# Kernel optimization log

Hardware: AMD Instinct MI355X
Metric: run time of the kernel (lower is better)

## Reference

```python
import jax, jax.numpy as jnp
import numpy as np

N_NODES = 40000
N_EDGES = 640000
IN, HID, OUT = 128, 256, 47


def setup_inputs() -> dict:
    key = jax.random.key(0)
    ks = jax.random.split(key, 8)
    x = jax.random.normal(ks[0], (N_NODES, IN), dtype=jnp.float32)
    # PyTorch Linear(fan_in, fan_out): store as [fan_in, fan_out] for y = h @ W + b
    W1 = jax.random.normal(ks[1], (2 * IN, HID), dtype=jnp.float32) / np.sqrt(2 * IN)
    b1 = jnp.zeros((HID,), jnp.float32)
    W2 = jax.random.normal(ks[2], (2 * HID, HID), dtype=jnp.float32) / np.sqrt(2 * HID)
    b2 = jnp.zeros((HID,), jnp.float32)
    W3 = jax.random.normal(ks[3], (2 * HID, OUT), dtype=jnp.float32) / np.sqrt(2 * HID)
    b3 = jnp.zeros((OUT,), jnp.float32)
    src = jax.random.randint(ks[4], (N_EDGES,), 0, N_NODES, dtype=jnp.int64 if jax.config.jax_enable_x64 else jnp.int32)
    dst = jax.random.randint(ks[5], (N_EDGES,), 0, N_NODES, dtype=jnp.int64 if jax.config.jax_enable_x64 else jnp.int32)
    return {"x": x, "W1": W1, "b1": b1, "W2": W2, "b2": b2, "W3": W3, "b3": b3,
            "src": src, "dst": dst}


def _sage_layer(h, src, dst, W, b):
    # copy_u -> mean: gather src features, scatter-sum into dst, divide by in-degree
    msum = jax.ops.segment_sum(h[src], dst, num_segments=N_NODES)  # [N, d]
    deg = jax.ops.segment_sum(jnp.ones_like(dst, dtype=h.dtype), dst, num_segments=N_NODES)
    mean = msum / jnp.maximum(deg, 1.0)[:, None]  # zero-degree nodes get 0 (DGL mean convention)
    cat = jnp.concatenate([h, mean], axis=1)      # [N, 2d]
    return cat @ W + b


def reference(x, W1, b1, W2, b2, W3, b3, src, dst):
    # dropout is identity in eval mode
    h = jax.nn.relu(_sage_layer(x, src, dst, W1, b1))
    h = jax.nn.relu(_sage_layer(h, src, dst, W2, b2))
    return _sage_layer(h, src, dst, W3, b3)
```

## Files before the change

kernel.cpp:

```cpp
#include <hip/hip_runtime.h>

#define NNODES 40000
#define NEDGES 640000
#define DIN 128
#define DHID 256
#define DOUT 47
#define NCNT 40960
#define NPART (NCNT / 256)

typedef __attribute__((ext_vector_type(8))) short short8;
typedef __attribute__((ext_vector_type(4))) float f32x4;

#define GLD16(gp, lp)                                                        \
    __builtin_amdgcn_global_load_lds(                                        \
        (const __attribute__((address_space(1))) void*)(gp),                 \
        (__attribute__((address_space(3))) void*)(lp), 16, 0, 0)

__device__ inline float bf2f(unsigned short u) {
    union { unsigned int i; float f; } c; c.i = ((unsigned int)u) << 16; return c.f;
}
__device__ inline unsigned short f2bf(float f) {
    union { float f; unsigned int i; } c; c.f = f;
    unsigned int x = c.i;
    x += 0x7fff + ((x >> 16) & 1);
    return (unsigned short)(x >> 16);
}

__global__ void hist_kernel(const int* __restrict__ dst, int* __restrict__ cnt) {
    int t = blockIdx.x * blockDim.x + threadIdx.x;
    if (t < NEDGES) atomicAdd(&cnt[dst[t]], 1);
}

__global__ void part_kernel(const int* __restrict__ cnt, int* __restrict__ part) {
    int b = blockIdx.x, t = threadIdx.x;
    int v = cnt[b * 256 + t];
#pragma unroll
    for (int off = 32; off > 0; off >>= 1) v += __shfl_down(v, off);
    __shared__ int ws[4];
    if ((t & 63) == 0) ws[t >> 6] = v;
    __syncthreads();
    if (t == 0) part[b] = ws[0] + ws[1] + ws[2] + ws[3];
}

__global__ void writeptr_kernel(const int* __restrict__ cnt, const int* __restrict__ part,
                                int* __restrict__ rowptr) {
    __shared__ int shp[256];
    __shared__ int sh[256];
    int b = blockIdx.x, t = threadIdx.x;
    int pv = (t < NPART) ? part[t] : 0;
    shp[t] = pv;
    __syncthreads();
    for (int off = 1; off < 256; off <<= 1) {
        int add = (t >= off) ? shp[t - off] : 0;
        __syncthreads();
        shp[t] += add;
        __syncthreads();
    }
    int partoff = (b == 0) ? 0 : shp[b - 1];
    int idx = b * 256 + t;
    int v = cnt[idx];
    sh[t] = v;
    __syncthreads();
    for (int off = 1; off < 256; off <<= 1) {
        int add = (t >= off) ? sh[t - off] : 0;
        __syncthreads();
        sh[t] += add;
        __syncthreads();
    }
    rowptr[idx] = partoff + sh[t] - v;
}

__global__ void fill_kernel(const int* __restrict__ src, const int* __restrict__ dst,
                            const int* __restrict__ rowptr, int* __restrict__ fill,
                            unsigned short* __restrict__ eidx) {
    int e = blockIdx.x * blockDim.x + threadIdx.x;
    if (e < NEDGES) {
        int d = dst[e];
        int pos = rowptr[d] + atomicAdd(&fill[d], 1);
        eidx[pos] = (unsigned short)src[e];
    }
}

__global__ void conv_all_kernel(const float* __restrict__ x,
                                const float* __restrict__ W1,
                                const float* __restrict__ W2,
                                const float* __restrict__ W3,
                                unsigned short* __restrict__ xbf,
                                unsigned short* __restrict__ wt1,
                                unsigned short* __restrict__ wt2,
                                unsigned short* __restrict__ wt3,
                                int* __restrict__ czero) {
    const int N0 = NNODES * DIN / 4;
    const int N1 = 2 * DIN * DHID;
    const int N2 = 2 * DHID * DHID;
    const int N3 = 94 * 256;
    int t = blockIdx.x * blockDim.x + threadIdx.x;
    if (t < 2 * NCNT) czero[t] = 0;
    if (t < N0) {
        float4 v = ((const float4*)x)[t];
        ushort4 r;
        r.x = f2bf(v.x); r.y = f2bf(v.y); r.z = f2bf(v.z); r.w = f2bf(v.w);
        ((ushort4*)xbf)[t] = r;
    } else if (t < N0 + N1) {
        int u = t - N0;
        int k = u >> 8, n = u & 255;
        wt1[(size_t)n * 256 + k] = f2bf(W1[u]);
    } else if (t < N0 + N1 + N2) {
        int u = t - N0 - N1;
        int k = u >> 8, n = u & 255;
        wt2[(size_t)n * 512 + k] = f2bf(W2[u]);
    } else if (t < N0 + N1 + N2 + N3) {
        int u = t - N0 - N1 - N2;
        int n = u >> 8, k = u & 255;
        float v = (n < 47) ? W3[(size_t)k * DOUT + n]
                           : W3[(size_t)(k + DHID) * DOUT + (n - 47)];
        wt3[u] = f2bf(v);
    }
}

template <int D>
__global__ void agg_bf16_kernel(const unsigned short* __restrict__ h,
                                const int* __restrict__ rowptr,
                                const unsigned short* __restrict__ eidx,
                                unsigned short* __restrict__ mean) {
    constexpr int VPL = D / 64;
    const int node = blockIdx.x * (blockDim.x >> 6) + (threadIdx.x >> 6);
    if (node >= NNODES) return;
    const int lane = threadIdx.x & 63;
    const int beg = rowptr[node], end = rowptr[node + 1];
    const unsigned short* hp = h + lane * VPL;

    float acc[VPL];
#pragma unroll
    for (int i = 0; i < VPL; ++i) acc[i] = 0.0f;

    for (int base = beg; base < end; base += 64) {
        int n = min(64, end - base);
        int myidx = (base + lane < end) ? (int)eidx[base + lane] : 0;
        int j = 0;
        for (; j + 8 <= n; j += 8) {
            int s[8];
#pragma unroll
            for (int u = 0; u < 8; ++u) s[u] = __shfl(myidx, j + u);
            if constexpr (VPL == 4) {
                ushort4 v[8];
#pragma unroll
                for (int u = 0; u < 8; ++u) v[u] = *(const ushort4*)(hp + (size_t)s[u] * D);
#pragma unroll
                for (int u = 0; u < 8; ++u) {
                    acc[0] += bf2f(v[u].x); acc[1] += bf2f(v[u].y);
                    acc[2] += bf2f(v[u].z); acc[3] += bf2f(v[u].w);
                }
            } else {
                ushort2 v[8];
#pragma unroll
                for (int u = 0; u < 8; ++u) v[u] = *(const ushort2*)(hp + (size_t)s[u] * D);
#pragma unroll
                for (int u = 0; u < 8; ++u) {
                    acc[0] += bf2f(v[u].x); acc[1] += bf2f(v[u].y);
                }
            }
        }
        for (; j + 4 <= n; j += 4) {
            int s[4];
#pragma unroll
            for (int u = 0; u < 4; ++u) s[u] = __shfl(myidx, j + u);
            if constexpr (VPL == 4) {
                ushort4 v[4];
#pragma unroll
                for (int u = 0; u < 4; ++u) v[u] = *(const ushort4*)(hp + (size_t)s[u] * D);
#pragma unroll
                for (int u = 0; u < 4; ++u) {
                    acc[0] += bf2f(v[u].x); acc[1] += bf2f(v[u].y);
                    acc[2] += bf2f(v[u].z); acc[3] += bf2f(v[u].w);
                }
            } else {
                ushort2 v[4];
#pragma unroll
                for (int u = 0; u < 4; ++u) v[u] = *(const ushort2*)(hp + (size_t)s[u] * D);
#pragma unroll
                for (int u = 0; u < 4; ++u) {
                    acc[0] += bf2f(v[u].x); acc[1] += bf2f(v[u].y);
                }
            }
        }
        for (; j < n; ++j) {
            int s = __shfl(myidx, j);
            if constexpr (VPL == 4) {
                ushort4 v = *(const ushort4*)(hp + (size_t)s * D);
                acc[0] += bf2f(v.x); acc[1] += bf2f(v.y);
                acc[2] += bf2f(v.z); acc[3] += bf2f(v.w);
            } else {
                ushort2 v = *(const ushort2*)(hp + (size_t)s * D);
                acc[0] += bf2f(v.x); acc[1] += bf2f(v.y);
            }
        }
    }
    float inv = (end > beg) ? 1.0f / (float)(end - beg) : 0.0f;
    unsigned short* o = mean + (size_t)node * D + lane * VPL;
    if constexpr (VPL == 4) {
        ushort4 r;
        r.x = f2bf(acc[0] * inv); r.y = f2bf(acc[1] * inv);
        r.z = f2bf(acc[2] * inv); r.w = f2bf(acc[3] * inv);
        *(ushort4*)o = r;
    } else {
        ushort2 r;
        r.x = f2bf(acc[0] * inv); r.y = f2bf(acc[1] * inv);
        *(ushort2*)o = r;
    }
}

__global__ void agg_p_kernel(const unsigned short* __restrict__ P,
                             const int* __restrict__ rowptr,
                             const unsigned short* __restrict__ eidx,
                             float* __restrict__ out) {
    const int node = blockIdx.x * (blockDim.x >> 6) + (threadIdx.x >> 6);
    if (node >= NNODES) return;
    const int lane = threadIdx.x & 63;
    const int beg = rowptr[node], end = rowptr[node + 1];
    const bool active = lane < 48;
    const int lc = active ? lane : 0;

    float acc = 0.0f;
    for (int base = beg; base < end; base += 64) {
        int n = min(64, end - base);
        int myidx = (base + lane < end) ? (int)eidx[base + lane] : 0;
        int j = 0;
        for (; j + 4 <= n; j += 4) {
            int s0 = __shfl(myidx, j);
            int s1 = __shfl(myidx, j + 1);
            int s2 = __shfl(myidx, j + 2);
            int s3 = __shfl(myidx, j + 3);
            if (active) {
                float a = bf2f(P[(size_t)s0 * 48 + lc]) + bf2f(P[(size_t)s1 * 48 + lc]);
                float b = bf2f(P[(size_t)s2 * 48 + lc]) + bf2f(P[(size_t)s3 * 48 + lc]);
                acc += a + b;
            }
        }
        for (; j < n; ++j) {
            int s = __shfl(myidx, j);
            if (active) acc += bf2f(P[(size_t)s * 48 + lc]);
        }
    }
    if (lane < 47 && end > beg) {
        out[(size_t)node * DOUT + lane] += acc / (float)(end - beg);
    }
}

template <int D>
__launch_bounds__(256, 2)
__global__ void gemm_fused_kernel(const unsigned short* __restrict__ H,
                                  const unsigned short* __restrict__ Mn,
                                  const unsigned short* __restrict__ Wt,
                                  const float* __restrict__ bias,
                                  unsigned short* __restrict__ hout) {
    constexpr int K = 2 * D;
    constexpr int NK = K / 32;
    __shared__ uint4 As4[2][64 * 4];
    __shared__ uint4 Bs4[2][256 * 4];

    const int tid = threadIdx.x;
    const int lane = tid & 63;
    const int w = tid >> 6;
    const int row0 = blockIdx.x * 64;

    const int lr = lane >> 2;
    const int lslot = lane & 3;
    const int swz = (lslot ^ ((lr >> 1) & 3)) * 8;
    const int arow = w * 16 + lr;
    const size_t abase = (size_t)(row0 + arow) * D;

    f32x4 acc[4][4];
#pragma unroll
    for (int m = 0; m < 4; ++m)
#pragma unroll
        for (int n = 0; n < 4; ++n) {
            f32x4 z = {0.0f, 0.0f, 0.0f, 0.0f};
            acc[m][n] = z;
        }

    const int fr = lane & 15;
    const int sl = lane >> 4;

    {
        GLD16(H + abase + swz, (char*)As4[0] + w * 1024);
#pragma unroll
        for (int c = 0; c < 4; ++c) {
            int brow = (w * 4 + c) * 16 + lr;
            GLD16(Wt + (size_t)brow * K + swz, (char*)Bs4[0] + (w * 4 + c) * 1024);
        }
    }
    __syncthreads();

#pragma unroll
    for (int t = 0; t < NK; ++t) {
        const int cur = t & 1;
        if (t + 1 < NK) {
            const int k0 = (t + 1) * 32;
            const unsigned short* ap = (k0 < D) ? (H + abase + k0 + swz)
                                                : (Mn + abase + (k0 - D) + swz);
            GLD16(ap, (char*)As4[cur ^ 1] + w * 1024);
#pragma unroll
            for (int c = 0; c < 4; ++c) {
                int brow = (w * 4 + c) * 16 + lr;
                GLD16(Wt + (size_t)brow * K + k0 + swz,
                      (char*)Bs4[cur ^ 1] + (w * 4 + c) * 1024);
            }
        }

        short8 af[4], bfv[4];
#pragma unroll
        for (int m = 0; m < 4; ++m) {
            int r = m * 16 + fr;
            union { uint4 u; short8 s; } cc;
            cc.u = As4[cur][r * 4 + (sl ^ ((r >> 1) & 3))];
            af[m] = cc.s;
        }
#pragma unroll
        for (int n = 0; n < 4; ++n) {
            int r = w * 64 + n * 16 + fr;
            union { uint4 u; short8 s; } cc;
            cc.u = Bs4[cur][r * 4 + (sl ^ ((r >> 1) & 3))];
            bfv[n] = cc.s;
        }
#pragma unroll
        for (int m = 0; m < 4; ++m)
#pragma unroll
            for (int n = 0; n < 4; ++n)
                acc[m][n] = __builtin_amdgcn_mfma_f32_16x16x32_bf16(af[m], bfv[n], acc[m][n], 0, 0, 0);

        __syncthreads();
    }

#pragma unroll
    for (int m = 0; m < 4; ++m) {
#pragma unroll
        for (int n = 0; n < 4; ++n) {
            int col = w * 64 + n * 16 + fr;
            float bv = bias[col];
#pragma unroll
            for (int q = 0; q < 4; ++q) {
                int row = row0 + m * 16 + sl * 4 + q;
                float v = fmaxf(acc[m][n][q] + bv, 0.0f);
                hout[(size_t)row * 256 + col] = f2bf(v);
            }
        }
    }
}

__launch_bounds__(256, 2)
__global__ void gemm3_kernel(const unsigned short* __restrict__ H,
                             const unsigned short* __restrict__ Wt,
                             const float* __restrict__ bias,
                             float* __restrict__ outp,
                             unsigned short* __restrict__ Pout,
                             int d, int N) {
    const int K = 2 * d;
    __shared__ uint4 AsB[128 * 4];
    __shared__ uint4 BsB[128 * 4];

    const int tid = threadIdx.x;
    const int lane = tid & 63;
    const int wid = tid >> 6;
    const int wr = wid >> 1, wc = wid & 1;
    const int row0 = blockIdx.x * 128;

    const int sr = tid >> 1;
    const int sh = tid & 1;
    const int gar = min(row0 + sr, NNODES - 1);
    const int gbr = min(sr, N - 1);
    const int ssw = (sr >> 1) & 3;

    f32x4 acc[4][4];
#pragma unroll
    for (int m = 0; m < 4; ++m)
#pragma unroll
        for (int n = 0; n < 4; ++n) {
            f32x4 z = {0.0f, 0.0f, 0.0f, 0.0f};
            acc[m][n] = z;
        }

    for (int k0 = 0; k0 < K; k0 += 32) {
        {
            const unsigned short* p = H + (size_t)gar * K + k0 + sh * 16;
            uint4 v0 = *(const uint4*)p;
            uint4 v1 = *(const uint4*)(p + 8);
            AsB[sr * 4 + ((2 * sh) ^ ssw)]     = v0;
            AsB[sr * 4 + ((2 * sh + 1) ^ ssw)] = v1;
        }
        {
            const unsigned short* p = Wt + (size_t)gbr * K + k0 + sh * 16;
            uint4 v0 = *(const uint4*)p;
            uint4 v1 = *(const uint4*)(p + 8);
            BsB[sr * 4 + ((2 * sh) ^ ssw)]     = v0;
            BsB[sr * 4 + ((2 * sh + 1) ^ ssw)] = v1;
        }
        __syncthreads();

        short8 af[4], bfv[4];
        const int fr = lane & 15;
        const int slot = lane >> 4;
#pragma unroll
        for (int m = 0; m < 4; ++m) {
            int r = wr * 64 + m * 16 + fr;
            union { uint4 u; short8 s; } cc;
            cc.u = AsB[r * 4 + (slot ^ ((r >> 1) & 3))];
            af[m] = cc.s;
        }
#pragma unroll
        for (int n = 0; n < 4; ++n) {
            int r = wc * 64 + n * 16 + fr;
            union { uint4 u; short8 s; } cc;
            cc.u = BsB[r * 4 + (slot ^ ((r >> 1) & 3))];
            bfv[n] = cc.s;
        }
#pragma unroll
        for (int m = 0; m < 4; ++m)
#pragma unroll
            for (int n = 0; n < 4; ++n)
                acc[m][n] = __builtin_amdgcn_mfma_f32_16x16x32_bf16(af[m], bfv[n], acc[m][n], 0, 0, 0);
        __syncthreads();
    }

#pragma unroll
    for (int m = 0; m < 4; ++m) {
#pragma unroll
        for (int n = 0; n < 4; ++n) {
            int col = wc * 64 + n * 16 + (lane & 15);
            if (col >= N) continue;
            float bv = (col < 47) ? bias[col] : 0.0f;
#pragma unroll
            for (int q = 0; q < 4; ++q) {
                int row = row0 + wr * 64 + m * 16 + (lane >> 4) * 4 + q;
                if (row < NNODES) {
                    float v = acc[m][n][q] + bv;
                    if (col < 47) outp[(size_t)row * DOUT + col] = v;
                    else Pout[(size_t)row * 48 + (col - 47)] = f2bf(v);
                }
            }
        }
    }
}

extern "C" void kernel_launch(void* const* d_in, const int* in_sizes, int n_in,
                              void* d_out, int out_size, void* d_ws, size_t ws_size,
                              hipStream_t stream) {
    const float* x  = (const float*)d_in[0];
    const float* W1 = (const float*)d_in[1];
    const float* b1 = (const float*)d_in[2];
    const float* W2 = (const float*)d_in[3];
    const float* b2 = (const float*)d_in[4];
    const float* W3 = (const float*)d_in[5];
    const float* b3 = (const float*)d_in[6];
    const int* src  = (const int*)d_in[7];
    const int* dst  = (const int*)d_in[8];
    float* out = (float*)d_out;

    int* rowptr  = (int*)d_ws;
    unsigned short* eidx = (unsigned short*)(rowptr + NCNT);
    int* cnt     = (int*)(eidx + NEDGES);
    int* fill    = cnt + NCNT;
    int* part    = fill + NCNT;
    unsigned short* xbf  = (unsigned short*)(part + 256);
    unsigned short* h1   = xbf + (size_t)NNODES * DIN;
    unsigned short* h2   = h1 + (size_t)NNODES * DHID;
    unsigned short* mean = h2 + (size_t)NNODES * DHID;
    unsigned short* wt1  = mean + (size_t)NNODES * DHID;
    unsigned short* wt2  = wt1 + 2 * DIN * DHID;
    unsigned short* wt3  = wt2 + 2 * DHID * DHID;
    unsigned short* P    = mean;

    {
        const int NT = NNODES * DIN / 4 + 2 * DIN * DHID + 2 * DHID * DHID + 94 * 256;
        conv_all_kernel<<<(NT + 255) / 256, 256, 0, stream>>>(x, W1, W2, W3, xbf, wt1, wt2, wt3, cnt);
    }

    hist_kernel<<<(NEDGES + 255) / 256, 256, 0, stream>>>(dst, cnt);
    part_kernel<<<NPART, 256, 0, stream>>>(cnt, part);
    writeptr_kernel<<<NPART, 256, 0, stream>>>(cnt, part, rowptr);
    fill_kernel<<<(NEDGES + 255) / 256, 256, 0, stream>>>(src, dst, rowptr, fill, eidx);

    agg_bf16_kernel<DIN><<<NNODES / 4, 256, 0, stream>>>(xbf, rowptr, eidx, mean);
    gemm_fused_kernel<DIN><<<NNODES / 64, 256, 0, stream>>>(xbf, mean, wt1, b1, h1);

    agg_bf16_kernel<DHID><<<NNODES / 4, 256, 0, stream>>>(h1, rowptr, eidx, mean);
    gemm_fused_kernel<DHID><<<NNODES / 64, 256, 0, stream>>>(h1, mean, wt2, b2, h2);

    gemm3_kernel<<<(NNODES + 127) / 128, 256, 0, stream>>>(h2, wt3, b3, out, P, DHID / 2, 94);
    agg_p_kernel<<<NNODES / 4, 256, 0, stream>>>(P, rowptr, eidx, out);
}
```

Before: 215.2 us.

## Fuse CSR build into cooperative kernel and vectorize final-layer aggregation

Replaces the four CSR construction kernels (histogram, partial sums, prefix scan, fill) with a single cooperative kernel that uses grid-wide syncs between phases, cutting three kernel launches and their gaps. The final-layer aggregation now has each wavefront split into four groups of 16 lanes. Each lane loads four bf16 features at once and handles a different edge, and the groups are combined with cross-lane shuffles at the end. Risks are the cost of the grid.sync calls, the need for all 640 blocks to be co-resident, and a different floating-point summation order.

```diff
diff --git a/kernel.cpp b/kernel.cpp
--- a/kernel.cpp
+++ b/kernel.cpp
@@ -1,4 +1,7 @@
 #include <hip/hip_runtime.h>
+#include <hip/hip_cooperative_groups.h>
+
+namespace cg = cooperative_groups;
 
 #define NNODES 40000
 #define NEDGES 640000
@@ -24,61 +27,6 @@
     unsigned int x = c.i;
     x += 0x7fff + ((x >> 16) & 1);
     return (unsigned short)(x >> 16);
-}
-
-__global__ void hist_kernel(const int* __restrict__ dst, int* __restrict__ cnt) {
-    int t = blockIdx.x * blockDim.x + threadIdx.x;
-    if (t < NEDGES) atomicAdd(&cnt[dst[t]], 1);
-}
-
-__global__ void part_kernel(const int* __restrict__ cnt, int* __restrict__ part) {
-    int b = blockIdx.x, t = threadIdx.x;
-    int v = cnt[b * 256 + t];
-#pragma unroll
-    for (int off = 32; off > 0; off >>= 1) v += __shfl_down(v, off);
-    __shared__ int ws[4];
-    if ((t & 63) == 0) ws[t >> 6] = v;
-    __syncthreads();
-    if (t == 0) part[b] = ws[0] + ws[1] + ws[2] + ws[3];
-}
-
-__global__ void writeptr_kernel(const int* __restrict__ cnt, const int* __restrict__ part,
-                                int* __restrict__ rowptr) {
-    __shared__ int shp[256];
-    __shared__ int sh[256];
-    int b = blockIdx.x, t = threadIdx.x;
-    int pv = (t < NPART) ? part[t] : 0;
-    shp[t] = pv;
-    __syncthreads();
-    for (int off = 1; off < 256; off <<= 1) {
-        int add = (t >= off) ? shp[t - off] : 0;
-        __syncthreads();
-        shp[t] += add;
-        __syncthreads();
-    }
-    int partoff = (b == 0) ? 0 : shp[b - 1];
-    int idx = b * 256 + t;
-    int v = cnt[idx];
-    sh[t] = v;
-    __syncthreads();
-    for (int off = 1; off < 256; off <<= 1) {
-        int add = (t >= off) ? sh[t - off] : 0;
-        __syncthreads();
-        sh[t] += add;
-        __syncthreads();
-    }
-    rowptr[idx] = partoff + sh[t] - v;
-}
-
-__global__ void fill_kernel(const int* __restrict__ src, const int* __restrict__ dst,
-                            const int* __restrict__ rowptr, int* __restrict__ fill,
-                            unsigned short* __restrict__ eidx) {
-    int e = blockIdx.x * blockDim.x + threadIdx.x;
-    if (e < NEDGES) {
-        int d = dst[e];
-        int pos = rowptr[d] + atomicAdd(&fill[d], 1);
-        eidx[pos] = (unsigned short)src[e];
-    }
 }
 
 __global__ void conv_all_kernel(const float* __restrict__ x,
@@ -118,6 +66,73 @@
     }
 }
 
+__global__ void csr_coop_kernel(const int* __restrict__ src,
+                                const int* __restrict__ dst,
+                                int* __restrict__ cnt,
+                                int* __restrict__ fill,
+                                int* __restrict__ part,
+                                int* __restrict__ partoff,
+                                int* __restrict__ rowptr,
+                                unsigned short* __restrict__ eidx) {
+    cg::grid_group grid = cg::this_grid();
+    const int nthr = gridDim.x * blockDim.x;
+    const int gtid = blockIdx.x * blockDim.x + threadIdx.x;
+
+    for (int e = gtid; e < NEDGES; e += nthr) atomicAdd(&cnt[dst[e]], 1);
+    grid.sync();
+
+    if (blockIdx.x < NPART) {
+        int b = blockIdx.x, t = threadIdx.x;
+        int v = cnt[b * 256 + t];
+#pragma unroll
+        for (int off = 32; off > 0; off >>= 1) v += __shfl_down(v, off);
+        __shared__ int ws4[4];
+        if ((t & 63) == 0) ws4[t >> 6] = v;
+        __syncthreads();
+        if (t == 0) part[b] = ws4[0] + ws4[1] + ws4[2] + ws4[3];
+    }
+    grid.sync();
+
+    if (blockIdx.x == 0) {
+        __shared__ int sh[256];
+        int t = threadIdx.x;
+        int v = (t < NPART) ? part[t] : 0;
+        sh[t] = v;
+        __syncthreads();
+        for (int off = 1; off < 256; off <<= 1) {
+            int add = (t >= off) ? sh[t - off] : 0;
+            __syncthreads();
+            sh[t] += add;
+            __syncthreads();
+        }
+        if (t < NPART) partoff[t] = sh[t] - v;
+    }
+    grid.sync();
+
+    if (blockIdx.x < NPART) {
+        __shared__ int sh2[256];
+        int b = blockIdx.x, t = threadIdx.x;
+        int idx = b * 256 + t;
+        int v = cnt[idx];
+        sh2[t] = v;
+        __syncthreads();
+        for (int off = 1; off < 256; off <<= 1) {
+            int add = (t >= off) ? sh2[t - off] : 0;
+            __syncthreads();
+            sh2[t] += add;
+            __syncthreads();
+        }
+        rowptr[idx] = partoff[b] + sh2[t] - v;
+    }
+    grid.sync();
+
+    for (int e = gtid; e < NEDGES; e += nthr) {
+        int d = dst[e];
+        int pos = rowptr[d] + atomicAdd(&fill[d], 1);
+        eidx[pos] = (unsigned short)src[e];
+    }
+}
+
 template <int D>
 __global__ void agg_bf16_kernel(const unsigned short* __restrict__ h,
                                 const int* __restrict__ rowptr,
@@ -217,33 +232,61 @@
     const int node = blockIdx.x * (blockDim.x >> 6) + (threadIdx.x >> 6);
     if (node >= NNODES) return;
     const int lane = threadIdx.x & 63;
+    const int g = lane >> 4;
+    const int f = lane & 15;
+    const bool af = f < 12;
     const int beg = rowptr[node], end = rowptr[node + 1];
-    const bool active = lane < 48;
-    const int lc = active ? lane : 0;
-
-    float acc = 0.0f;
+    const unsigned short* pp = P + f * 4;
+
+    float a0 = 0.0f, a1 = 0.0f, a2 = 0.0f, a3 = 0.0f;
     for (int base = beg; base < end; base += 64) {
         int n = min(64, end - base);
         int myidx = (base + lane < end) ? (int)eidx[base + lane] : 0;
         int j = 0;
+        for (; j + 16 <= n; j += 16) {
+            int s0 = __shfl(myidx, j + g);
+            int s1 = __shfl(myidx, j + 4 + g);
+            int s2 = __shfl(myidx, j + 8 + g);
+            int s3 = __shfl(myidx, j + 12 + g);
+            if (af) {
+                ushort4 v0 = *(const ushort4*)(pp + (size_t)s0 * 48);
+                ushort4 v1 = *(const ushort4*)(pp + (size_t)s1 * 48);
+                ushort4 v2 = *(const ushort4*)(pp + (size_t)s2 * 48);
+                ushort4 v3 = *(const ushort4*)(pp + (size_t)s3 * 48);
+                a0 += (bf2f(v0.x) + bf2f(v1.x)) + (bf2f(v2.x) + bf2f(v3.x));
+                a1 += (bf2f(v0.y) + bf2f(v1.y)) + (bf2f(v2.y) + bf2f(v3.y));
+                a2 += (bf2f(v0.z) + bf2f(v1.z)) + (bf2f(v2.z) + bf2f(v3.z));
+                a3 += (bf2f(v0.w) + bf2f(v1.w)) + (bf2f(v2.w) + bf2f(v3.w));
+            }
+        }
         for (; j + 4 <= n; j += 4) {
-            int s0 = __shfl(myidx, j);
-            int s1 = __shfl(myidx, j + 1);
-            int s2 = __shfl(myidx, j + 2);
-            int s3 = __shfl(myidx, j + 3);
-            if (active) {
-                float a = bf2f(P[(size_t)s0 * 48 + lc]) + bf2f(P[(size_t)s1 * 48 + lc]);
-                float b = bf2f(P[(size_t)s2 * 48 + lc]) + bf2f(P[(size_t)s3 * 48 + lc]);
-                acc += a + b;
-            }
-        }
-        for (; j < n; ++j) {
-            int s = __shfl(myidx, j);
-            if (active) acc += bf2f(P[(size_t)s * 48 + lc]);
-        }
-    }
-    if (lane < 47 && end > beg) {
-        out[(size_t)node * DOUT + lane] += acc / (float)(end - beg);
+            int s0 = __shfl(myidx, j + g);
+            if (af) {
+                ushort4 v0 = *(const ushort4*)(pp + (size_t)s0 * 48);
+                a0 += bf2f(v0.x); a1 += bf2f(v0.y);
+                a2 += bf2f(v0.z); a3 += bf2f(v0.w);
+            }
+        }
+        int rem = n - j;
+        int srcl = (g < rem) ? (j + g) : 0;
+        int s0 = __shfl(myidx, srcl);
+        if (g < rem && af) {
+            ushort4 v0 = *(const ushort4*)(pp + (size_t)s0 * 48);
+            a0 += bf2f(v0.x); a1 += bf2f(v0.y);
+            a2 += bf2f(v0.z); a3 += bf2f(v0.w);
+        }
+    }
+    a0 += __shfl_xor(a0, 16); a1 += __shfl_xor(a1, 16);
+    a2 += __shfl_xor(a2, 16); a3 += __shfl_xor(a3, 16);
+    a0 += __shfl_xor(a0, 32); a1 += __shfl_xor(a1, 32);
+    a2 += __shfl_xor(a2, 32); a3 += __shfl_xor(a3, 32);
+    if (lane < 12 && end > beg) {
+        float inv = 1.0f / (float)(end - beg);
+        float* o = out + (size_t)node * DOUT + lane * 4;
+        o[0] += a0 * inv;
+        o[1] += a1 * inv;
+        o[2] += a2 * inv;
+        if (lane * 4 + 3 < DOUT) o[3] += a3 * inv;
     }
 }
 
@@ -461,7 +504,8 @@
     int* cnt     = (int*)(eidx + NEDGES);
     int* fill    = cnt + NCNT;
     int* part    = fill + NCNT;
-    unsigned short* xbf  = (unsigned short*)(part + 256);
+    int* partoff = part + 256;
+    unsigned short* xbf  = (unsigned short*)(partoff + 256);
     unsigned short* h1   = xbf + (size_t)NNODES * DIN;
     unsigned short* h2   = h1 + (size_t)NNODES * DHID;
     unsigned short* mean = h2 + (size_t)NNODES * DHID;
@@ -475,10 +519,20 @@
         conv_all_kernel<<<(NT + 255) / 256, 256, 0, stream>>>(x, W1, W2, W3, xbf, wt1, wt2, wt3, cnt);
     }
 
-    hist_kernel<<<(NEDGES + 255) / 256, 256, 0, stream>>>(dst, cnt);
-    part_kernel<<<NPART, 256, 0, stream>>>(cnt, part);
-    writeptr_kernel<<<NPART, 256, 0, stream>>>(cnt, part, rowptr);
-    fill_kernel<<<(NEDGES + 255) / 256, 256, 0, stream>>>(src, dst, rowptr, fill, eidx);
+    {
+        const int* srcA = src;
+        const int* dstA = dst;
+        int* cntA = cnt;
+        int* fillA = fill;
+        int* partA = part;
+        int* partoffA = partoff;
+        int* rowptrA = rowptr;
+        unsigned short* eidxA = eidx;
+        void* args[] = {(void*)&srcA, (void*)&dstA, (void*)&cntA, (void*)&fillA,
+                        (void*)&partA, (void*)&partoffA, (void*)&rowptrA, (void*)&eidxA};
+        hipLaunchCooperativeKernel((const void*)csr_coop_kernel, dim3(640), dim3(256),
+                                   args, 0, stream);
+    }
 
     agg_bf16_kernel<DIN><<<NNODES / 4, 256, 0, stream>>>(xbf, rowptr, eidx, mean);
     gemm_fused_kernel<DIN><<<NNODES / 64, 256, 0, stream>>>(xbf, mean, wt1, b1, h1);
```

New measurement: 484.6 us. 125% more time.
